# Performance work log

Measured on AMD Instinct MI355X. Metric: run time of the kernel, lower is better.

## Reference

```python
import jax, jax.numpy as jnp
import numpy as np

EPS = 1e-5


def _forward(fov, motion, video, timewindow,
             gru_w_ih, gru_w_hh, gru_b_ih, gru_b_hh,
             Wp, Wv_w, Wv_b, Wpv_w, Wpv_b,
             conv_w, conv_b, vbn_g, vbn_b,
             me_w, me_b, mbn_g, mbn_b):
    B, S, _ = fov.shape
    P = timewindow.shape[0]
    tot = B * S * P
    H = 784

    # ---- GRU (batch_first, 1 layer), PyTorch gate order r,z,n ----
    def step(h, x):  # h,x: [B,H],[B,528]
        gi = x @ gru_w_ih.T + gru_b_ih            # [B,3H]
        gh = h @ gru_w_hh.T + gru_b_hh
        i_r, i_z, i_n = jnp.split(gi, 3, axis=-1)
        h_r, h_z, h_n = jnp.split(gh, 3, axis=-1)
        r = jax.nn.sigmoid(i_r + h_r)
        z = jax.nn.sigmoid(i_z + h_z)
        n = jnp.tanh(i_n + r * h_n)
        h_new = (1.0 - z) * n + z * h
        return h_new, h_new

    h0 = jnp.zeros((B, H), dtype=fov.dtype)
    _, pref_seq = jax.lax.scan(step, h0, jnp.swapaxes(fov, 0, 1))  # [S,B,H]
    preference = jnp.swapaxes(pref_seq, 0, 1)                       # [B,S,H]

    # expand over P predictions -> [tot, 784]
    preference = jnp.broadcast_to(preference[:, :, None, :], (B, S, P, H)).reshape(tot, H)

    # ---- additive (Bahdanau) attention over 196 spatial locations ----
    p_att = preference @ Wp.T                                       # [tot,128]
    # attention keys: view video buffer as (tot,528,196), transpose
    v_key = jnp.swapaxes(video.reshape(tot, 528, 196), -2, -1)      # [tot,196,528]
    v_att = jnp.einsum('tnc,mc->tnm', v_key, Wv_w) + Wv_b           # [tot,196,128]
    v_att = jnp.tanh(v_att + p_att[:, None, :])
    scores = jnp.einsum('tnm,om->tno', v_att, Wpv_w)[..., 0] + Wpv_b[0]  # [tot,196]
    att = jax.nn.softmax(scores, axis=1)[..., None]                 # [tot,196,1]

    # weighted sum path: SAME buffer reinterpreted as (tot,196,528) (faithful to torch .view)
    vid = video.reshape(tot, 196, 528) * att                        # [tot,196,528]
    vid = jnp.swapaxes(vid, -2, -1)                                 # [tot,528,196]

    # 1x1 conv (528->4) + BatchNorm2d (batch stats) + ReLU
    vid = jnp.einsum('oc,tcn->ton', conv_w[:, :, 0, 0], vid) + conv_b[None, :, None]  # [tot,4,196]
    mu = jnp.mean(vid, axis=(0, 2), keepdims=True)
    var = jnp.var(vid, axis=(0, 2), keepdims=True)
    vid = (vid - mu) * jax.lax.rsqrt(var + EPS) * vbn_g[None, :, None] + vbn_b[None, :, None]
    vid = jax.nn.relu(vid).reshape(tot, 4 * 196)                    # [tot,784]

    # ---- motion branch: expand over P, Linear(90,128) + BatchNorm1d + ReLU ----
    mot = jnp.broadcast_to(motion[:, :, None, :, :], (B, S, P, 1, 90)).reshape(tot, 90)
    mot = mot @ me_w.T + me_b                                       # [tot,128]
    mmu = jnp.mean(mot, axis=0, keepdims=True)
    mvar = jnp.var(mot, axis=0, keepdims=True)
    mot = (mot - mmu) * jax.lax.rsqrt(mvar + EPS) * mbn_g + mbn_b
    mot = jax.nn.relu(mot)                                          # [tot,128]

    tw = jnp.broadcast_to(timewindow[None, :], (B * S, P)).reshape(tot, 1)
    return jnp.concatenate([tw, preference, mot, vid], axis=1)      # [tot,1697]


def setup_inputs() -> dict:
    key = jax.random.key(0)
    ks = jax.random.split(key, 24)
    B, S, P = 8, 32, 5
    C, H, M = 528, 784, 128

    def rn(k, shape, scale=0.05):
        return jax.random.normal(k, shape, dtype=jnp.float32) * scale

    return {
        'fov': rn(ks[0], (B, S, C), 1.0),
        'motion': rn(ks[1], (B, S, 1, 90), 1.0),
        'video': rn(ks[2], (B, S, P, C, 196), 1.0),
        'timewindow': jnp.arange(1, P + 1, dtype=jnp.float32),
        'gru_w_ih': rn(ks[3], (3 * H, C)),
        'gru_w_hh': rn(ks[4], (3 * H, H)),
        'gru_b_ih': rn(ks[5], (3 * H,)),
        'gru_b_hh': rn(ks[6], (3 * H,)),
        'Wp': rn(ks[7], (M, H)),
        'Wv_w': rn(ks[8], (M, C)),
        'Wv_b': rn(ks[9], (M,)),
        'Wpv_w': rn(ks[10], (1, M)),
        'Wpv_b': rn(ks[11], (1,)),
        'conv_w': rn(ks[12], (4, C, 1, 1)),
        'conv_b': rn(ks[13], (4,)),
        'vbn_g': jnp.ones((4,), jnp.float32),
        'vbn_b': jnp.zeros((4,), jnp.float32),
        'me_w': rn(ks[14], (M, 90)),
        'me_b': rn(ks[15], (M,)),
        'mbn_g': jnp.ones((M,), jnp.float32),
        'mbn_b': jnp.zeros((M,), jnp.float32),
    }


def reference(fov, motion, video, timewindow,
              gru_w_ih, gru_w_hh, gru_b_ih, gru_b_hh,
              Wp, Wv_w, Wv_b, Wpv_w, Wpv_b,
              conv_w, conv_b, vbn_g, vbn_b,
              me_w, me_b, mbn_g, mbn_b):
    return _forward(fov, motion, video, timewindow,
                    gru_w_ih, gru_w_hh, gru_b_ih, gru_b_hh,
                    Wp, Wv_w, Wv_b, Wpv_w, Wpv_b,
                    conv_w, conv_b, vbn_g, vbn_b,
                    me_w, me_b, mbn_g, mbn_b)
```

## Files before the change

### kernel.cpp

```cpp
#include <hip/hip_runtime.h>
#include <cfloat>
#include <cmath>


typedef __attribute__((ext_vector_type(8))) short short8;
typedef __attribute__((ext_vector_type(4))) float f32x4;

__device__ __forceinline__ unsigned bf16r(float f) {
  union { float f; unsigned u; } v;
  v.f = f;
  unsigned u = v.u;
  u += 0x7fffu + ((u >> 16) & 1u);
  return u >> 16;
}

__device__ __forceinline__ short8 pack8(const float* f) {
  short8 r;
#pragma unroll
  for (int j = 0; j < 8; ++j) r[j] = (short)bf16r(f[j]);
  return r;
}

__device__ __forceinline__ float tanh_fast(float x) {
  float e = __expf(2.f * x);
  return 1.f - 2.f / (e + 1.f);
}

#define GT_BM 32
#define GT_BN 64
#define GT_BK 16

__global__ __launch_bounds__(256) void gemm_nt(const float* __restrict__ A,
                                               const float* __restrict__ Bt,
                                               const float* __restrict__ bias,
                                               float* __restrict__ Cm,
                                               int Mn, int Nn, int Kn) {
  __shared__ float sA[GT_BM][GT_BK + 1];
  __shared__ float sB[GT_BK][68];
  const int tid = threadIdx.x;
  const int tm = tid >> 4;
  const int tn = tid & 15;
  const int rowBase = blockIdx.y * GT_BM;
  const int colBase = blockIdx.x * GT_BN;
  float acc[2][4] = {};

  for (int k0 = 0; k0 < Kn; k0 += GT_BK) {
    for (int u = tid; u < GT_BM * GT_BK; u += 256) {
      int r = u >> 4, kk = u & 15;
      int gk = k0 + kk, gr = rowBase + r;
      sA[r][kk] = (gr < Mn && gk < Kn) ? A[(size_t)gr * Kn + gk] : 0.f;
    }
    for (int u = tid; u < GT_BN * GT_BK; u += 256) {
      int n = u >> 4, kk = u & 15;
      int gk = k0 + kk, gn = colBase + n;
      sB[kk][n] = (gn < Nn && gk < Kn) ? Bt[(size_t)gn * Kn + gk] : 0.f;
    }
    __syncthreads();
#pragma unroll
    for (int kk = 0; kk < GT_BK; ++kk) {
      float a0 = sA[tm * 2 + 0][kk];
      float a1 = sA[tm * 2 + 1][kk];
      float b0 = sB[kk][tn * 4 + 0];
      float b1 = sB[kk][tn * 4 + 1];
      float b2 = sB[kk][tn * 4 + 2];
      float b3 = sB[kk][tn * 4 + 3];
      acc[0][0] += a0 * b0; acc[0][1] += a0 * b1; acc[0][2] += a0 * b2; acc[0][3] += a0 * b3;
      acc[1][0] += a1 * b0; acc[1][1] += a1 * b1; acc[1][2] += a1 * b2; acc[1][3] += a1 * b3;
    }
    __syncthreads();
  }
#pragma unroll
  for (int i = 0; i < 2; ++i)
#pragma unroll
    for (int j = 0; j < 4; ++j) {
      int gr = rowBase + tm * 2 + i;
      int gc = colBase + tn * 4 + j;
      if (gr < Mn && gc < Nn) {
        float v = acc[i][j];
        if (bias) v += bias[gc];
        Cm[(size_t)gr * Nn + gc] = v;
      }
    }
}

__global__ __launch_bounds__(256) void whh_transpose(const float* __restrict__ W,
                                                     float* __restrict__ WT) {
  __shared__ float tile[32][33];
  const int n0 = blockIdx.x * 32;
  const int k0 = blockIdx.y * 32;
  const int tx = threadIdx.x & 31;
  const int ty = threadIdx.x >> 5;
  for (int i = ty; i < 32; i += 8) {
    int n = n0 + i, k = k0 + tx;
    tile[i][tx] = (n < 2352 && k < 784) ? W[(size_t)n * 784 + k] : 0.f;
  }
  __syncthreads();
  for (int i = ty; i < 32; i += 8) {
    int k = k0 + i, n = n0 + tx;
    if (k < 784 && n < 2352) WT[(size_t)k * 2352 + n] = tile[tx][i];
  }
}

__global__ __launch_bounds__(256) void gru_dots(const float* __restrict__ WT,
                                                const float* __restrict__ h,
                                                float* __restrict__ gh) {
  __shared__ float sh[4 * 784];
  const int tid = threadIdx.x;
  const int bh = blockIdx.y;
  const int bloc = tid >> 6;
  const int b = bh * 4 + bloc;
  const int n = blockIdx.x * 64 + (tid & 63);
  for (int u = tid; u < 3136; u += 256) sh[u] = h[bh * 3136 + u];
  __syncthreads();
  if (n >= 2352) return;
  const float4* h4 = (const float4*)(sh + bloc * 784);
  const float* wp = WT + n;
  float acc = 0.f;
#pragma unroll 2
  for (int kk = 0; kk < 196; ++kk) {
    float4 hv = h4[kk];
    const float* w = wp + (size_t)(kk * 4) * 2352;
    acc += hv.x * w[0];
    acc += hv.y * w[2352];
    acc += hv.z * w[4704];
    acc += hv.w * w[7056];
  }
  gh[b * 2352 + n] = acc;
}

__global__ __launch_bounds__(256) void gru_combine(const float* __restrict__ GI,
                                                   const float* __restrict__ gh,
                                                   const float* __restrict__ bhh,
                                                   const float* __restrict__ h_in,
                                                   float* __restrict__ h_out,
                                                   float* __restrict__ pref,
                                                   int s) {
  const int g = blockIdx.x * 256 + threadIdx.x;
  if (g >= 6272) return;
  const int b = g / 784;
  const int j = g - b * 784;
  const int bs = b * 32 + s;
  const float* gi = GI + (size_t)bs * 2352;
  const float* ghb = gh + b * 2352;
  float ghr = ghb[j] + bhh[j];
  float ghz = ghb[784 + j] + bhh[784 + j];
  float ghn = ghb[1568 + j] + bhh[1568 + j];
  float r = 1.f / (1.f + __expf(-(gi[j] + ghr)));
  float z = 1.f / (1.f + __expf(-(gi[784 + j] + ghz)));
  float nn = tanh_fast(gi[1568 + j] + r * ghn);
  float hn = (1.f - z) * nn + z * h_in[g];
  h_out[g] = hn;
  pref[(size_t)bs * 784 + j] = hn;
}

__global__ __launch_bounds__(128) void mot_stats(const float* __restrict__ mot,
                                                 float* __restrict__ msum,
                                                 float* __restrict__ msq) {
  int m = threadIdx.x;
  float s = 0.f, q = 0.f;
  for (int r = 0; r < 256; ++r) {
    float v = mot[r * 128 + m];
    s += v;
    q += v * v;
  }
  msum[m] = s;
  msq[m] = q;
}

struct AttnP1 { short sA[128 * 40]; short sB[224 * 40]; };
struct AttnP2 { float red[256]; float pre[784]; };
union AttnU { AttnP1 p1; AttnP2 p2; };

__global__ __launch_bounds__(256, 2) void attn_fused(
    const float* __restrict__ video, const float* __restrict__ Wv,
    const float* __restrict__ Wvb, const float* __restrict__ patt,
    const float* __restrict__ Wpv, const float* __restrict__ convw,
    const float* __restrict__ convb, float* __restrict__ vid_pre,
    float* __restrict__ vstats) {
  __shared__ AttnU u;
  __shared__ float pa[128];
  __shared__ float wpv[128];
  __shared__ float ssc[224];

  const int t = blockIdx.x;
  const int bs = t / 5;
  const int tid = threadIdx.x;
  const int wave = tid >> 6;
  const int lane = tid & 63;
  const int q = lane >> 4;
  const int ln = lane & 15;
  const int wm = wave >> 1;
  const int wn = wave & 1;

  if (tid < 128) {
    pa[tid] = Wvb[tid] + patt[(size_t)bs * 128 + tid];
    wpv[tid] = Wpv[tid];
  }
  if (tid < 224) ssc[tid] = 0.f;

  f32x4 acc[4][7];
#pragma unroll
  for (int i = 0; i < 4; ++i)
#pragma unroll
    for (int j = 0; j < 7; ++j) acc[i][j] = (f32x4){0.f, 0.f, 0.f, 0.f};

  const float* vbase = video + (size_t)t * 103488;

  for (int c0 = 0; c0 < 544; c0 += 32) {
    for (int uu = tid; uu < 2048; uu += 256) {
      int m = uu >> 4, p = uu & 15;
      int c = c0 + 2 * p;
      float f0 = (c < 528) ? Wv[m * 528 + c] : 0.f;
      float f1 = (c + 1 < 528) ? Wv[m * 528 + c + 1] : 0.f;
      unsigned pack = bf16r(f0) | (bf16r(f1) << 16);
      *(unsigned*)&u.p1.sA[m * 40 + 2 * p] = pack;
    }
    for (int uu = tid; uu < 3584; uu += 256) {
      int p = uu / 224;
      int n = uu - p * 224;
      int c = c0 + 2 * p;
      float f0 = 0.f, f1 = 0.f;
      if (n < 196) {
        if (c < 528) f0 = vbase[(size_t)c * 196 + n];
        if (c + 1 < 528) f1 = vbase[(size_t)(c + 1) * 196 + n];
      }
      unsigned pack = bf16r(f0) | (bf16r(f1) << 16);
      int pc = p ^ ((n & 3) << 2);
      *(unsigned*)&u.p1.sB[n * 40 + 2 * pc] = pack;
    }
    __syncthreads();

    short8 afr[4], bfr[7];
#pragma unroll
    for (int mi = 0; mi < 4; ++mi) {
      int m = wm * 64 + mi * 16 + ln;
      afr[mi] = *(const short8*)&u.p1.sA[m * 40 + q * 8];
    }
#pragma unroll
    for (int nj = 0; nj < 7; ++nj) {
      int n = wn * 112 + nj * 16 + ln;
      int p0 = (q * 4) ^ ((n & 3) << 2);
      bfr[nj] = *(const short8*)&u.p1.sB[n * 40 + 2 * p0];
    }
#pragma unroll
    for (int mi = 0; mi < 4; ++mi)
#pragma unroll
      for (int nj = 0; nj < 7; ++nj)
        acc[mi][nj] = __builtin_amdgcn_mfma_f32_16x16x32_bf16(
            afr[mi], bfr[nj], acc[mi][nj], 0, 0, 0);
    __syncthreads();
  }

  float contrib[7] = {};
#pragma unroll
  for (int mi = 0; mi < 4; ++mi)
#pragma unroll
    for (int r = 0; r < 4; ++r) {
      int m = wm * 64 + mi * 16 + q * 4 + r;
      float w = wpv[m];
      float bia = pa[m];
#pragma unroll
      for (int nj = 0; nj < 7; ++nj)
        contrib[nj] += w * tanh_fast(acc[mi][nj][r] + bia);
    }
#pragma unroll
  for (int nj = 0; nj < 7; ++nj)
    atomicAdd(&ssc[wn * 112 + nj * 16 + ln], contrib[nj]);
  __syncthreads();

  float v = (tid < 196) ? ssc[tid] : -FLT_MAX;
  u.p2.red[tid] = v;
  __syncthreads();
  for (int st = 128; st > 0; st >>= 1) {
    if (tid < st) u.p2.red[tid] = fmaxf(u.p2.red[tid], u.p2.red[tid + st]);
    __syncthreads();
  }
  float mx = u.p2.red[0];
  __syncthreads();
  float e = (tid < 196) ? __expf(v - mx) : 0.f;
  u.p2.red[tid] = e;
  __syncthreads();
  for (int st = 128; st > 0; st >>= 1) {
    if (tid < st) u.p2.red[tid] += u.p2.red[tid + st];
    __syncthreads();
  }
  float tot = u.p2.red[0];
  __syncthreads();
  if (tid < 196) ssc[tid] = e / tot;
  __syncthreads();

  short8 aw[17];
#pragma unroll
  for (int k = 0; k < 17; ++k) {
    float fa[8];
#pragma unroll
    for (int j = 0; j < 8; ++j) {
      int c = k * 32 + q * 8 + j;
      fa[j] = (ln < 4 && c < 528) ? convw[ln * 528 + c] : 0.f;
    }
    aw[k] = pack8(fa);
  }

  for (int tile = wave; tile < 13; tile += 4) {
    int n = tile * 16 + ln;
    bool nv = (n < 196);
    const float* vp = vbase + (size_t)n * 528;
    f32x4 cc = (f32x4){0.f, 0.f, 0.f, 0.f};
#pragma unroll
    for (int k = 0; k < 17; ++k) {
      int c0 = k * 32 + q * 8;
      short8 bf;
      if (nv && c0 + 7 < 528) {
        float4 v0 = *(const float4*)(vp + c0);
        float4 v1 = *(const float4*)(vp + c0 + 4);
        float fb[8] = {v0.x, v0.y, v0.z, v0.w, v1.x, v1.y, v1.z, v1.w};
        bf = pack8(fb);
      } else {
        bf = (short8){0, 0, 0, 0, 0, 0, 0, 0};
      }
      cc = __builtin_amdgcn_mfma_f32_16x16x32_bf16(aw[k], bf, cc, 0, 0, 0);
    }
    if (q == 0 && nv) {
      float a = ssc[n];
#pragma unroll
      for (int r = 0; r < 4; ++r)
        u.p2.pre[r * 196 + n] = a * cc[r] + convb[r];
    }
  }
  __syncthreads();

  float ls[4] = {0.f, 0.f, 0.f, 0.f};
  float lq[4] = {0.f, 0.f, 0.f, 0.f};
  for (int uu = tid; uu < 784; uu += 256) {
    float x = u.p2.pre[uu];
    vid_pre[(size_t)t * 784 + uu] = x;
    int o = uu / 196;
#pragma unroll
    for (int oo = 0; oo < 4; ++oo) {
      ls[oo] += (o == oo) ? x : 0.f;
      lq[oo] += (o == oo) ? x * x : 0.f;
    }
  }
#pragma unroll
  for (int oo = 0; oo < 4; ++oo)
#pragma unroll
    for (int off = 32; off > 0; off >>= 1) {
      ls[oo] += __shfl_down(ls[oo], off);
      lq[oo] += __shfl_down(lq[oo], off);
    }
  if (lane == 0)
#pragma unroll
    for (int oo = 0; oo < 4; ++oo) {
      atomicAdd(&vstats[oo], ls[oo]);
      atomicAdd(&vstats[4 + oo], lq[oo]);
    }
}

__global__ __launch_bounds__(256) void finalize(
    const float* __restrict__ tw, const float* __restrict__ prefb,
    const float* __restrict__ motl, const float* __restrict__ msum,
    const float* __restrict__ msq, const float* __restrict__ mg,
    const float* __restrict__ mb, const float* __restrict__ vid_pre,
    const float* __restrict__ vstats, const float* __restrict__ vg,
    const float* __restrict__ vbb, float* __restrict__ out) {
  int g = blockIdx.x * 256 + threadIdx.x;
  if (g >= 1280 * 1697) return;
  int t = g / 1697;
  int col = g - t * 1697;
  int bs = t / 5;
  int p = t - bs * 5;
  float r;
  if (col == 0) {
    r = tw[p];
  } else if (col < 785) {
    r = prefb[(size_t)bs * 784 + (col - 1)];
  } else if (col < 913) {
    int m = col - 785;
    float x = motl[(size_t)bs * 128 + m];
    float mu = msum[m] * (1.f / 256.f);
    float var = msq[m] * (1.f / 256.f) - mu * mu;
    float y = (x - mu) * rsqrtf(var + 1e-5f) * mg[m] + mb[m];
    r = fmaxf(y, 0.f);
  } else {
    int qd = col - 913;
    int o = qd / 196;
    float x = vid_pre[(size_t)t * 784 + qd];
    float mu = vstats[o] * (1.f / 250880.f);
    float var = vstats[4 + o] * (1.f / 250880.f) - mu * mu;
    float y = (x - mu) * rsqrtf(var + 1e-5f) * vg[o] + vbb[o];
    r = fmaxf(y, 0.f);
  }
  out[g] = r;
}

extern "C" void kernel_launch(void* const* d_in, const int* in_sizes, int n_in,
                              void* d_out, int out_size, void* d_ws,
                              size_t ws_size, hipStream_t stream) {
  const float* fov = (const float*)d_in[0];
  const float* motion = (const float*)d_in[1];
  const float* video = (const float*)d_in[2];
  const float* timew = (const float*)d_in[3];
  const float* w_ih = (const float*)d_in[4];
  const float* w_hh = (const float*)d_in[5];
  const float* b_ih = (const float*)d_in[6];
  const float* b_hh = (const float*)d_in[7];
  const float* Wp = (const float*)d_in[8];
  const float* Wv_w = (const float*)d_in[9];
  const float* Wv_b = (const float*)d_in[10];
  const float* Wpv_w = (const float*)d_in[11];
  const float* Wpv_b = (const float*)d_in[12];
  const float* conv_w = (const float*)d_in[13];
  const float* conv_b = (const float*)d_in[14];
  const float* vbn_g = (const float*)d_in[15];
  const float* vbn_b = (const float*)d_in[16];
  const float* me_w = (const float*)d_in[17];
  const float* me_b = (const float*)d_in[18];
  const float* mbn_g = (const float*)d_in[19];
  const float* mbn_b = (const float*)d_in[20];
  (void)Wpv_b;

  float* ws = (float*)d_ws;
  float* h0b = ws + 0;
  float* stats = ws + 6272;
  float* msum = stats;
  float* msq = stats + 128;
  float* vstats = stats + 256;
  float* h1b = ws + 6656;
  float* gh = ws + 12928;
  float* GI = ws + 31744;
  float* prefb = ws + 633856;
  float* patt = ws + 834560;
  float* motl = ws + 867328;
  float* vid_pre = ws + 1150976;
  float* WT = ws + 2154496;

  hipMemsetAsync(ws, 0, 6536 * sizeof(float), stream);

  whh_transpose<<<dim3(74, 25), 256, 0, stream>>>(w_hh, WT);

  gemm_nt<<<dim3((2352 + GT_BN - 1) / GT_BN, 256 / GT_BM), 256, 0, stream>>>(
      fov, w_ih, b_ih, GI, 256, 2352, 528);

  for (int s = 0; s < 32; ++s) {
    const float* hin = (s & 1) ? h1b : h0b;
    float* hout = (s & 1) ? h0b : h1b;
    gru_dots<<<dim3(37, 2), 256, 0, stream>>>(WT, hin, gh);
    gru_combine<<<25, 256, 0, stream>>>(GI, gh, b_hh, hin, hout, prefb, s);
  }

  gemm_nt<<<dim3(2, 8), 256, 0, stream>>>(prefb, Wp, nullptr, patt, 256, 128, 784);
  gemm_nt<<<dim3(2, 8), 256, 0, stream>>>(motion, me_w, me_b, motl, 256, 128, 90);
  mot_stats<<<1, 128, 0, stream>>>(motl, msum, msq);

  attn_fused<<<1280, 256, 0, stream>>>(video, Wv_w, Wv_b, patt, Wpv_w, conv_w,
                                       conv_b, vid_pre, vstats);

  int total = 1280 * 1697;
  finalize<<<(total + 255) / 256, 256, 0, stream>>>(
      timew, prefb, motl, msum, msq, mbn_g, mbn_b, vid_pre, vstats, vbn_g,
      vbn_b, (float*)d_out);
}
```

Baseline: 2.928 ms.

## Widen attention kernel to 512 threads and load 8-channel bf16 packs per thread

Doubles the attn_fused block to 512 threads (8 waves). Each wave now covers a 32x112 MFMA tile instead of 64x112, so the accumulator state per thread halves and more waves can be resident. The LDS fill loops are rewritten so each thread loads 8 consecutive channels and stores one short8, replacing the 2-element packed stores. The XOR swizzle on the video tile is dropped, which may bring back LDS bank conflicts. The softmax and epilogue loops are adjusted for the larger block, and the reduction writes are guarded to tid<256.

```diff
diff --git a/kernel.cpp b/kernel.cpp
--- a/kernel.cpp
+++ b/kernel.cpp
@@ -171,7 +171,7 @@
 struct AttnP2 { float red[256]; float pre[784]; };
 union AttnU { AttnP1 p1; AttnP2 p2; };
 
-__global__ __launch_bounds__(256, 2) void attn_fused(
+__global__ __launch_bounds__(512, 4) void attn_fused(
     const float* __restrict__ video, const float* __restrict__ Wv,
     const float* __restrict__ Wvb, const float* __restrict__ patt,
     const float* __restrict__ Wpv, const float* __restrict__ convw,
@@ -198,52 +198,59 @@
   }
   if (tid < 224) ssc[tid] = 0.f;
 
-  f32x4 acc[4][7];
-#pragma unroll
-  for (int i = 0; i < 4; ++i)
+  f32x4 acc[2][7];
+#pragma unroll
+  for (int i = 0; i < 2; ++i)
 #pragma unroll
     for (int j = 0; j < 7; ++j) acc[i][j] = (f32x4){0.f, 0.f, 0.f, 0.f};
 
   const float* vbase = video + (size_t)t * 103488;
 
   for (int c0 = 0; c0 < 544; c0 += 32) {
-    for (int uu = tid; uu < 2048; uu += 256) {
-      int m = uu >> 4, p = uu & 15;
-      int c = c0 + 2 * p;
-      float f0 = (c < 528) ? Wv[m * 528 + c] : 0.f;
-      float f1 = (c + 1 < 528) ? Wv[m * 528 + c + 1] : 0.f;
-      unsigned pack = bf16r(f0) | (bf16r(f1) << 16);
-      *(unsigned*)&u.p1.sA[m * 40 + 2 * p] = pack;
-    }
-    for (int uu = tid; uu < 3584; uu += 256) {
-      int p = uu / 224;
-      int n = uu - p * 224;
-      int c = c0 + 2 * p;
-      float f0 = 0.f, f1 = 0.f;
+    {
+      int m = tid >> 2;
+      int g = tid & 3;
+      int cb = c0 + g * 8;
+      float f[8];
+#pragma unroll
+      for (int j = 0; j < 8; ++j) {
+        int c = cb + j;
+        f[j] = (c < 528) ? Wv[m * 528 + c] : 0.f;
+      }
+      *(short8*)&u.p1.sA[m * 40 + g * 8] = pack8(f);
+    }
+    for (int uu = tid; uu < 896; uu += 512) {
+      int g = uu / 224;
+      int n = uu - g * 224;
+      int cb = c0 + g * 8;
+      float f[8];
       if (n < 196) {
-        if (c < 528) f0 = vbase[(size_t)c * 196 + n];
-        if (c + 1 < 528) f1 = vbase[(size_t)(c + 1) * 196 + n];
+#pragma unroll
+        for (int j = 0; j < 8; ++j) {
+          int c = cb + j;
+          f[j] = (c < 528) ? vbase[(size_t)c * 196 + n] : 0.f;
+        }
+      } else {
+#pragma unroll
+        for (int j = 0; j < 8; ++j) f[j] = 0.f;
       }
-      unsigned pack = bf16r(f0) | (bf16r(f1) << 16);
-      int pc = p ^ ((n & 3) << 2);
-      *(unsigned*)&u.p1.sB[n * 40 + 2 * pc] = pack;
-    }
-    __syncthreads();
-
-    short8 afr[4], bfr[7];
-#pragma unroll
-    for (int mi = 0; mi < 4; ++mi) {
-      int m = wm * 64 + mi * 16 + ln;
+      *(short8*)&u.p1.sB[n * 40 + g * 8] = pack8(f);
+    }
+    __syncthreads();
+
+    short8 afr[2], bfr[7];
+#pragma unroll
+    for (int mi = 0; mi < 2; ++mi) {
+      int m = wm * 32 + mi * 16 + ln;
       afr[mi] = *(const short8*)&u.p1.sA[m * 40 + q * 8];
     }
 #pragma unroll
     for (int nj = 0; nj < 7; ++nj) {
       int n = wn * 112 + nj * 16 + ln;
-      int p0 = (q * 4) ^ ((n & 3) << 2);
-      bfr[nj] = *(const short8*)&u.p1.sB[n * 40 + 2 * p0];
-    }
-#pragma unroll
-    for (int mi = 0; mi < 4; ++mi)
+      bfr[nj] = *(const short8*)&u.p1.sB[n * 40 + q * 8];
+    }
+#pragma unroll
+    for (int mi = 0; mi < 2; ++mi)
 #pragma unroll
       for (int nj = 0; nj < 7; ++nj)
         acc[mi][nj] = __builtin_amdgcn_mfma_f32_16x16x32_bf16(
@@ -253,10 +260,10 @@
 
   float contrib[7] = {};
 #pragma unroll
-  for (int mi = 0; mi < 4; ++mi)
+  for (int mi = 0; mi < 2; ++mi)
 #pragma unroll
     for (int r = 0; r < 4; ++r) {
-      int m = wm * 64 + mi * 16 + q * 4 + r;
+      int m = wm * 32 + mi * 16 + q * 4 + r;
       float w = wpv[m];
       float bia = pa[m];
 #pragma unroll
@@ -269,7 +276,7 @@
   __syncthreads();
 
   float v = (tid < 196) ? ssc[tid] : -FLT_MAX;
-  u.p2.red[tid] = v;
+  if (tid < 256) u.p2.red[tid] = v;
   __syncthreads();
   for (int st = 128; st > 0; st >>= 1) {
     if (tid < st) u.p2.red[tid] = fmaxf(u.p2.red[tid], u.p2.red[tid + st]);
@@ -278,7 +285,7 @@
   float mx = u.p2.red[0];
   __syncthreads();
   float e = (tid < 196) ? __expf(v - mx) : 0.f;
-  u.p2.red[tid] = e;
+  if (tid < 256) u.p2.red[tid] = e;
   __syncthreads();
   for (int st = 128; st > 0; st >>= 1) {
     if (tid < st) u.p2.red[tid] += u.p2.red[tid + st];
@@ -301,7 +308,7 @@
     aw[k] = pack8(fa);
   }
 
-  for (int tile = wave; tile < 13; tile += 4) {
+  for (int tile = wave; tile < 13; tile += 8) {
     int n = tile * 16 + ln;
     bool nv = (n < 196);
     const float* vp = vbase + (size_t)n * 528;
@@ -331,7 +338,7 @@
 
   float ls[4] = {0.f, 0.f, 0.f, 0.f};
   float lq[4] = {0.f, 0.f, 0.f, 0.f};
-  for (int uu = tid; uu < 784; uu += 256) {
+  for (int uu = tid; uu < 784; uu += 512) {
     float x = u.p2.pre[uu];
     vid_pre[(size_t)t * 784 + uu] = x;
     int o = uu / 196;
@@ -452,7 +459,7 @@
   gemm_nt<<<dim3(2, 8), 256, 0, stream>>>(motion, me_w, me_b, motl, 256, 128, 90);
   mot_stats<<<1, 128, 0, stream>>>(motl, msum, msq);
 
-  attn_fused<<<1280, 256, 0, stream>>>(video, Wv_w, Wv_b, patt, Wpv_w, conv_w,
+  attn_fused<<<1280, 512, 0, stream>>>(video, Wv_w, Wv_b, patt, Wpv_w, conv_w,
                                        conv_b, vid_pre, vstats);
 
   int total = 1280 * 1697;
```

Measured after the change: 3.112 ms. +6.3%, slower.
